# Kernel tuning notes

Measured on AMD Instinct MI355X. Metric: run time of the kernel, lower is better.

Reference implementation:

```python
import jax, jax.numpy as jnp
import numpy as np

B, N, E = 8, 64, 192
D_IN, D_PROJ = 1024, 256
F = 16            # cfg.NGM.GNN_FEAT per layer
SK_TAU = 0.05     # cfg.NGM.SK_TAU
SK_ITERS = 10
BIN_ITERS = 10
NN = N * N


def _project(x, Wp, bp, gamma, beta):
    # self.projection: Linear(1024,256) -> BatchNorm1d(256) (batch stats) -> ReLU
    B_, M, _ = x.shape
    h = x.reshape(B_ * M, -1) @ Wp + bp
    mu = h.mean(0)
    var = h.var(0)
    h = (h - mu) / jnp.sqrt(var + 1e-5) * gamma + beta
    return jax.nn.relu(h).reshape(B_, M, -1)


def _l2n(x):
    return x / jnp.clip(jnp.linalg.norm(x, axis=-1, keepdims=True), 1e-12)


def _log_sinkhorn(log_s, iters):
    for _ in range(iters):
        log_s = log_s - jax.nn.logsumexp(log_s, axis=2, keepdims=True)
        log_s = log_s - jax.nn.logsumexp(log_s, axis=1, keepdims=True)
    return jnp.exp(log_s)


def _build_K(Ke, Kp, s1, d1, s2, d2):
    # construct_sparse_aff_mat: K[a2*N+a1, b2*N+b1] += Ke[e1, e2]
    rows = s2[None, :] * N + s1[:, None]      # [E, E]
    cols = d2[None, :] * N + d1[:, None]      # [E, E]
    flat = (rows.astype(jnp.int32) * NN + cols.astype(jnp.int32)).ravel()
    K = jnp.zeros((NN * NN,), Ke.dtype).at[flat].add(Ke.ravel()).reshape(NN, NN)
    diag = jnp.arange(NN)
    # diagonal holds vec(Kp^T) (ordering a2*N + a1, matching emb = Kp.T.reshape(-1,1))
    return K.at[diag, diag].set(Kp.T.ravel())


def setup_inputs() -> dict:
    key = jax.random.key(0)
    ks = jax.random.split(key, 32)
    inp = {}
    inp['x1'] = jax.random.normal(ks[0], (B, N, D_IN), jnp.float32)
    inp['x2'] = jax.random.normal(ks[1], (B, N, D_IN), jnp.float32)
    inp['e1'] = jax.random.normal(ks[2], (B, E, D_IN), jnp.float32)
    inp['e2'] = jax.random.normal(ks[3], (B, E, D_IN), jnp.float32)
    inp['Wp'] = jax.random.normal(ks[4], (D_IN, D_PROJ), jnp.float32) * 0.02
    inp['bp'] = jnp.zeros((D_PROJ,), jnp.float32)
    inp['gamma'] = jnp.ones((D_PROJ,), jnp.float32)
    inp['beta'] = jnp.zeros((D_PROJ,), jnp.float32)
    in_dims = [1, F + 1, F + 1]
    for i, din in enumerate(in_dims):
        inp[f'W{i}'] = jax.random.normal(ks[5 + 3 * i], (din, F), jnp.float32) * 0.2
        inp[f'b{i}'] = jnp.zeros((F,), jnp.float32)
        inp[f'S{i}'] = jax.random.normal(ks[6 + 3 * i], (F, 1), jnp.float32) * 0.2
        inp[f'c{i}'] = jnp.zeros((1,), jnp.float32)
    inp['Wc'] = jax.random.normal(ks[20], (F + 1, 1), jnp.float32) * 0.2
    inp['bc'] = jnp.zeros((1,), jnp.float32)
    inp['bin_value'] = jnp.ones((1,), jnp.float32) * 0.2
    inp['src1'] = jax.random.randint(ks[21], (B, E), 0, N, jnp.int32)
    inp['dst1'] = jax.random.randint(ks[22], (B, E), 0, N, jnp.int32)
    inp['src2'] = jax.random.randint(ks[23], (B, E), 0, N, jnp.int32)
    inp['dst2'] = jax.random.randint(ks[24], (B, E), 0, N, jnp.int32)
    return inp


def reference(x1, x2, e1, e2, Wp, bp, gamma, beta,
              W0, b0, S0, c0, W1, b1, S1, c1, W2, b2, S2, c2,
              Wc, bc, bin_value, src1, dst1, src2, dst2):
    # unary / quadratic affinities via projected, L2-normalized inner products
    p1 = _project(x1, Wp, bp, gamma, beta)
    p2 = _project(x2, Wp, bp, gamma, beta)
    q1 = _project(e1, Wp, bp, gamma, beta)
    q2 = _project(e2, Wp, bp, gamma, beta)
    Kp = jnp.einsum('bnd,bmd->bnm', _l2n(p1), _l2n(p2))        # [B, N1, N2]
    Ke = 0.5 * jnp.einsum('bed,bfd->bef', _l2n(q1), _l2n(q2))  # [B, E1, E2]
    # sparse Kronecker affinity assembled densely (association graph adjacency)
    K = jax.vmap(_build_K)(Ke, Kp, src1, dst1, src2, dst2)     # [B, NN, NN]
    A = (K > 0).astype(K.dtype)
    deg = jnp.clip(A.sum(-1), 1.0)                              # [B, NN]
    x = Kp.transpose(0, 2, 1).reshape(B, NN, 1)                 # emb = vec(Kp^T)
    for (W, b, S, c) in ((W0, b0, S0, c0), (W1, b1, S1, c1), (W2, b2, S2, c2)):
        msg = jnp.einsum('bij,bjc->bic', K, x) / deg[..., None]  # sparse matvec (memory-bound)
        h = jax.nn.relu(msg @ W + b)                             # [B, NN, F]
        v = (h @ S + c).reshape(B, N, N)                         # row order a2*N+a1 -> [B, N2, N1]
        ss = _log_sinkhorn(v.transpose(0, 2, 1) / SK_TAU, SK_ITERS)  # Sinkhorn embedding channel
        x = jnp.concatenate([h, ss.transpose(0, 2, 1).reshape(B, NN, 1)], -1)
    v = (x @ Wc + bc).reshape(B, N, N)
    s = v.transpose(0, 2, 1)                                    # [B, N1, N2]
    # BinSinkhorn: pad with learned bin value, dual normalization, strip bin
    binv = bin_value[0]
    ls = jnp.concatenate([s, jnp.full((B, 1, N), binv, s.dtype)], 1)
    ls = jnp.concatenate([ls, jnp.full((B, N + 1, 1), binv, s.dtype)], 2)
    P = _log_sinkhorn(ls, BIN_ITERS)
    ss = P[:, :N, :N]
    return ss / jax.lax.stop_gradient(ss.max())
```

## Files before the change

### kernel.cpp

```cpp
#include <hip/hip_runtime.h>

constexpr int kB   = 8;
constexpr int kN   = 64;
constexpr int kE   = 192;
constexpr int kDin = 1024;
constexpr int kDp  = 256;
constexpr int kNN  = 4096;
constexpr float kTauInv = 20.0f;
constexpr int kXS  = 16;

typedef float vfloat4 __attribute__((ext_vector_type(4)));

struct SmemGemm { float As[2][16][68]; float Ws[2][16][68]; };
struct SmemCsr  {
    int km1[4096], km2[4096];
    short es1[kE], es2[kE], rp1[kE], rp2[kE];
    int cnt1[64], cnt2[64], pos1[64], pos2[64];
    int ccnt1[kE], ccnt2[kE], cpos1[kE], cpos2[kE];
};
union __align__(16) SmemK1 { SmemGemm g; SmemCsr csr; };

__global__ __launch_bounds__(256) void k_projcsr(
    const float* __restrict__ x1, const float* __restrict__ x2,
    const float* __restrict__ e1, const float* __restrict__ e2,
    const float* __restrict__ Wp,
    const int* __restrict__ src1, const int* __restrict__ dst1,
    const int* __restrict__ src2, const int* __restrict__ dst2,
    float* __restrict__ P, float* __restrict__ stats,
    int* __restrict__ off1, int* __restrict__ off2,
    int* __restrict__ lst1, int* __restrict__ lst2,
    int* __restrict__ rep1g, int* __restrict__ rep2g,
    int* __restrict__ coff1, int* __restrict__ coff2,
    int* __restrict__ clst1, int* __restrict__ clst2)
{
    const int bid = blockIdx.x, t = threadIdx.x;
    __shared__ SmemK1 u;

    if (bid < 1024) {
        const int xcd = bid & 7;
        const int ct = (bid >> 3) & 3;
        const int p = (bid >> 5) * 8 + xcd;
        const int z = p >> 6;
        const int rt = p & 63;
        const int grow0 = rt * 64, col0 = ct * 64;
        const float* src; int lrow0;
        if (rt < 8)       { src = x1; lrow0 = grow0; }
        else if (rt < 16) { src = x2; lrow0 = grow0 - 512; }
        else if (rt < 40) { src = e1; lrow0 = grow0 - 1024; }
        else              { src = e2; lrow0 = grow0 - 2560; }

        const int tx = t & 15, ty = t >> 4;
        const int arow = t >> 2, acol = (t & 3) * 4;
        const int wrow = t >> 4, wcol = (t & 15) * 4;

        const float* Abase = src + (size_t)(lrow0 + arow) * kDin + z * 256 + acol;
        const float* Wbase = Wp + (size_t)(z * 256 + wrow) * kDp + col0 + wcol;

        float4 a4 = *(const float4*)Abase;
        float4 w4 = *(const float4*)Wbase;
        float acc[4][4] = {};

        for (int c = 0; c < 16; ++c) {
            const int cur = c & 1;
            u.g.As[cur][acol + 0][arow] = a4.x;
            u.g.As[cur][acol + 1][arow] = a4.y;
            u.g.As[cur][acol + 2][arow] = a4.z;
            u.g.As[cur][acol + 3][arow] = a4.w;
            *(float4*)&u.g.Ws[cur][wrow][wcol] = w4;
            __syncthreads();
            if (c < 15) {
                a4 = *(const float4*)(Abase + (c + 1) * 16);
                w4 = *(const float4*)(Wbase + (size_t)(c + 1) * 16 * kDp);
            }
#pragma unroll
            for (int kk = 0; kk < 16; ++kk) {
                float4 av = *(const float4*)&u.g.As[cur][kk][ty * 4];
                float4 wv = *(const float4*)&u.g.Ws[cur][kk][tx * 4];
                float a[4] = {av.x, av.y, av.z, av.w};
                float w[4] = {wv.x, wv.y, wv.z, wv.w};
#pragma unroll
                for (int i = 0; i < 4; ++i)
#pragma unroll
                    for (int j = 0; j < 4; ++j)
                        acc[i][j] += a[i] * w[j];
            }
        }
        float* Pz = P + (size_t)z * 1048576;
#pragma unroll
        for (int i = 0; i < 4; ++i) {
            const int row = grow0 + ty * 4 + i;
            float4 v;
            v.x = acc[i][0]; v.y = acc[i][1]; v.z = acc[i][2]; v.w = acc[i][3];
            *(float4*)&Pz[(size_t)row * kDp + col0 + tx * 4] = v;
        }
    } else {
        const int b = bid - 1024;
        auto& C = u.csr;
        if (b == 0)
            for (int i = t; i < 2048; i += 256) stats[i] = 0.f;
        for (int i = t; i < 4096; i += 256) {
            C.km1[i] = 0x7fffffff; C.km2[i] = 0x7fffffff;
        }
        if (t < 64) { C.cnt1[t] = 0; C.cnt2[t] = 0; }
        for (int i = t; i < kE; i += 256) { C.ccnt1[i] = 0; C.ccnt2[i] = 0; }
        __syncthreads();
        if (t < kE) {
            int v1 = src1[b * kE + t], v2 = src2[b * kE + t];
            C.es1[t] = (short)v1; C.es2[t] = (short)v2;
            atomicAdd(&C.cnt1[v1], 1);
            atomicAdd(&C.cnt2[v2], 1);
            atomicMin(&C.km1[v1 * 64 + dst1[b * kE + t]], t);
            atomicMin(&C.km2[v2 * 64 + dst2[b * kE + t]], t);
        }
        __syncthreads();
        if (t < kE) {
            int r1 = C.km1[C.es1[t] * 64 + dst1[b * kE + t]];
            int r2 = C.km2[C.es2[t] * 64 + dst2[b * kE + t]];
            C.rp1[t] = (short)r1; C.rp2[t] = (short)r2;
            rep1g[b * kE + t] = r1; rep2g[b * kE + t] = r2;
            atomicAdd(&C.ccnt1[r1], 1);
            atomicAdd(&C.ccnt2[r2], 1);
        }
        __syncthreads();
        if (t == 0) {
            int a = 0, c = 0;
            for (int v = 0; v < 64; ++v) { C.pos1[v] = a; a += C.cnt1[v]; C.pos2[v] = c; c += C.cnt2[v]; }
            a = 0; c = 0;
            for (int v = 0; v < kE; ++v) { C.cpos1[v] = a; a += C.ccnt1[v]; C.cpos2[v] = c; c += C.ccnt2[v]; }
        }
        __syncthreads();
        if (t < 64) { off1[b * 65 + t] = C.pos1[t]; off2[b * 65 + t] = C.pos2[t]; }
        if (t == 0) { off1[b * 65 + 64] = kE; off2[b * 65 + 64] = kE; }
        if (t < kE) { coff1[b * 193 + t] = C.cpos1[t]; coff2[b * 193 + t] = C.cpos2[t]; }
        if (t == 0) { coff1[b * 193 + kE] = kE; coff2[b * 193 + kE] = kE; }
        __syncthreads();
        if (t < kE) {
            int p = atomicAdd(&C.pos1[C.es1[t]], 1); lst1[b * kE + p] = t;
            int q = atomicAdd(&C.pos2[C.es2[t]], 1); lst2[b * kE + q] = t;
            int cp = atomicAdd(&C.cpos1[C.rp1[t]], 1); clst1[b * kE + cp] = t;
            int cq = atomicAdd(&C.cpos2[C.rp2[t]], 1); clst2[b * kE + cq] = t;
        }
    }
}

__global__ __launch_bounds__(256) void k_reduce(
    const float* __restrict__ P, const float* __restrict__ bp,
    float* __restrict__ hbuf, float* __restrict__ stats)
{
    const int t = threadIdx.x;
    const int r0 = blockIdx.x * 16;
    const int seg = (r0 < 512) ? 0 : (r0 < 1024 ? 1 : (r0 < 2560 ? 2 : 3));
    const float bb = bp[t];
    float s = 0.f, s2 = 0.f;
#pragma unroll
    for (int rr = 0; rr < 16; ++rr) {
        size_t o = (size_t)(r0 + rr) * kDp + t;
        float v = P[o] + P[o + 1048576] + P[o + 2097152] + P[o + 3145728] + bb;
        hbuf[o] = v;
        s += v; s2 += v * v;
    }
    atomicAdd(&stats[seg * 512 + t], s);
    atomicAdd(&stats[seg * 512 + 256 + t], s2);
}

struct __align__(16) SmemSim  {
    float Xs[32][36]; float Ys[32][36];
    float muX[256], isX[256], muY[256], isY[256];
    float ga[256], be[256];
    float scX[32], scY[32];
};

__global__ __launch_bounds__(256) void k_sim(
    const float* __restrict__ hbuf, const float* __restrict__ stats,
    const float* __restrict__ gamma, const float* __restrict__ beta,
    float* __restrict__ Kp, float* __restrict__ Ke,
    int* __restrict__ bars)
{
    const int bid = blockIdx.x, t = threadIdx.x;
    __shared__ SmemSim u;

    if (bid == 0 && t == 0) { bars[3584] = 0; bars[3600] = 0; }

    const int id = bid % 40, b = bid / 40;
    int mt, nt_, ldo, segX, segY, xrow0, yrow0; float* outp; float scale;
    if (id < 4) {
        mt = (id >> 1) * 32; nt_ = (id & 1) * 32; ldo = 64;
        xrow0 = b * 64; yrow0 = 512 + b * 64;
        segX = 0; segY = 1;
        outp = Kp + (size_t)b * 4096; scale = 1.0f;
    } else {
        int e = id - 4;
        mt = (e / 6) * 32; nt_ = (e % 6) * 32; ldo = 192;
        xrow0 = 1024 + b * 192; yrow0 = 2560 + b * 192;
        segX = 2; segY = 3;
        outp = Ke + (size_t)b * 36864; scale = 0.5f;
    }
    {
        const float n = (segX < 2) ? 512.f : 1536.f;
        float mu = stats[segX * 512 + t] / n;
        float var = stats[segX * 512 + 256 + t] / n - mu * mu;
        u.muX[t] = mu; u.isX[t] = rsqrtf(var + 1e-5f);
        mu = stats[segY * 512 + t] / n;
        var = stats[segY * 512 + 256 + t] / n - mu * mu;
        u.muY[t] = mu; u.isY[t] = rsqrtf(var + 1e-5f);
        u.ga[t] = gamma[t]; u.be[t] = beta[t];
    }
    __syncthreads();
    {
        const int ri = t >> 2, lane = t & 3;
        const bool isXr = ri < 32;
        const int grow = isXr ? (xrow0 + mt + ri) : (yrow0 + nt_ + (ri - 32));
        const float* mus = isXr ? u.muX : u.muY;
        const float* iss = isXr ? u.isX : u.isY;
        const float* hr = hbuf + (size_t)grow * kDp;
        float ss = 0.f;
        for (int c4 = 0; c4 < 16; ++c4) {
            int c = lane * 64 + c4 * 4;
            float4 v = *(const float4*)&hr[c];
            float p;
            p = fmaxf((v.x - mus[c+0]) * iss[c+0] * u.ga[c+0] + u.be[c+0], 0.f); ss += p * p;
            p = fmaxf((v.y - mus[c+1]) * iss[c+1] * u.ga[c+1] + u.be[c+1], 0.f); ss += p * p;
            p = fmaxf((v.z - mus[c+2]) * iss[c+2] * u.ga[c+2] + u.be[c+2], 0.f); ss += p * p;
            p = fmaxf((v.w - mus[c+3]) * iss[c+3] * u.ga[c+3] + u.be[c+3], 0.f); ss += p * p;
        }
        ss += __shfl_xor(ss, 1);
        ss += __shfl_xor(ss, 2);
        if (lane == 0) {
            float sc = 1.f / fmaxf(sqrtf(ss), 1e-12f);
            if (isXr) u.scX[ri] = sc; else u.scY[ri - 32] = sc;
        }
    }
    __syncthreads();
    const int row = t >> 3, kq = t & 7;
    const int ty = t >> 4, tx = t & 15;
    const float* Xp = hbuf + (size_t)(xrow0 + mt) * kDp;
    const float* Yp = hbuf + (size_t)(yrow0 + nt_) * kDp;
    float acc[2][2] = {};
    for (int k0 = 0; k0 < kDp; k0 += 32) {
        const int c = k0 + kq * 4;
        float4 xa = *(const float4*)(Xp + (size_t)row * kDp + c);
        float4 ya = *(const float4*)(Yp + (size_t)row * kDp + c);
        const float sx = u.scX[row], sy = u.scY[row];
        u.Xs[kq*4+0][row] = fmaxf((xa.x - u.muX[c+0]) * u.isX[c+0] * u.ga[c+0] + u.be[c+0], 0.f) * sx;
        u.Xs[kq*4+1][row] = fmaxf((xa.y - u.muX[c+1]) * u.isX[c+1] * u.ga[c+1] + u.be[c+1], 0.f) * sx;
        u.Xs[kq*4+2][row] = fmaxf((xa.z - u.muX[c+2]) * u.isX[c+2] * u.ga[c+2] + u.be[c+2], 0.f) * sx;
        u.Xs[kq*4+3][row] = fmaxf((xa.w - u.muX[c+3]) * u.isX[c+3] * u.ga[c+3] + u.be[c+3], 0.f) * sx;
        u.Ys[kq*4+0][row] = fmaxf((ya.x - u.muY[c+0]) * u.isY[c+0] * u.ga[c+0] + u.be[c+0], 0.f) * sy;
        u.Ys[kq*4+1][row] = fmaxf((ya.y - u.muY[c+1]) * u.isY[c+1] * u.ga[c+1] + u.be[c+1], 0.f) * sy;
        u.Ys[kq*4+2][row] = fmaxf((ya.z - u.muY[c+2]) * u.isY[c+2] * u.ga[c+2] + u.be[c+2], 0.f) * sy;
        u.Ys[kq*4+3][row] = fmaxf((ya.w - u.muY[c+3]) * u.isY[c+3] * u.ga[c+3] + u.be[c+3], 0.f) * sy;
        __syncthreads();
#pragma unroll
        for (int kk = 0; kk < 32; ++kk) {
            float2 xv = *(const float2*)&u.Xs[kk][ty * 2];
            float2 yv = *(const float2*)&u.Ys[kk][tx * 2];
            acc[0][0] += xv.x * yv.x; acc[0][1] += xv.x * yv.y;
            acc[1][0] += xv.y * yv.x; acc[1][1] += xv.y * yv.y;
        }
        __syncthreads();
    }
#pragma unroll
    for (int i = 0; i < 2; ++i)
#pragma unroll
        for (int j = 0; j < 2; ++j)
            outp[(size_t)(mt + ty * 2 + i) * ldo + nt_ + tx * 2 + j] = scale * acc[i][j];
}

struct __align__(16) SmemLayer {
    float mat[64][68]; float fL[64], gL[64];
    float WL[17 * 16]; float bL[16], SL[16]; float c0v;
    float WcL[17];
    int jd2[kE]; int il[kE]; float msgT[64][18];
    int co1L[kE + 1], co2L[kE + 1];
    short cl1L[kE], cl2L[kE];
};

__device__ void sink64_local(int b, int t, float (*mat)[68], float* fL, float* gL,
                             const float* __restrict__ vin)
{
    const float4* v4 = (const float4*)(vin + b * kNN);
    for (int i = t; i < 1024; i += 256) {
        float4 v = v4[i];
        int idx = i * 4;
        int q = idx >> 6, p = idx & 63;
        mat[p][q]     = v.x * kTauInv;
        mat[p + 1][q] = v.y * kTauInv;
        mat[p + 2][q] = v.z * kTauInv;
        mat[p + 3][q] = v.w * kTauInv;
    }
    if (t < 64) { fL[t] = 0.f; gL[t] = 0.f; }
    __syncthreads();
    const int r = t >> 2, s = t & 3;
    float tv[16];
    for (int it = 0; it < 10; ++it) {
        float mx = -1e30f;
#pragma unroll
        for (int k = 0; k < 16; ++k) {
            float v = mat[r][s + 4 * k] + gL[s + 4 * k];
            tv[k] = v; mx = fmaxf(mx, v);
        }
        mx = fmaxf(mx, __shfl_xor(mx, 1));
        mx = fmaxf(mx, __shfl_xor(mx, 2));
        float sum = 0.f;
#pragma unroll
        for (int k = 0; k < 16; ++k) sum += __expf(tv[k] - mx);
        sum += __shfl_xor(sum, 1);
        sum += __shfl_xor(sum, 2);
        if (s == 0) fL[r] = -(mx + __logf(sum));
        __syncthreads();
        mx = -1e30f;
#pragma unroll
        for (int k = 0; k < 16; ++k) {
            float v = mat[s + 4 * k][r] + fL[s + 4 * k];
            tv[k] = v; mx = fmaxf(mx, v);
        }
        mx = fmaxf(mx, __shfl_xor(mx, 1));
        mx = fmaxf(mx, __shfl_xor(mx, 2));
        sum = 0.f;
#pragma unroll
        for (int k = 0; k < 16; ++k) sum += __expf(tv[k] - mx);
        sum += __shfl_xor(sum, 1);
        sum += __shfl_xor(sum, 2);
        if (s == 0) gL[r] = -(mx + __logf(sum));
        __syncthreads();
    }
    const float fr = fL[r];
#pragma unroll
    for (int k = 0; k < 16; ++k) {
        int q = s + 4 * k;
        mat[r][q] = __expf(mat[r][q] + fr + gL[q]);
    }
    __syncthreads();
}

template <int C, bool LASTP>
__device__ void layer_body(int bid, int t, SmemLayer& L,
    const int* __restrict__ off1, const int* __restrict__ lst1,
    const int* __restrict__ off2, const int* __restrict__ lst2,
    const int* __restrict__ d1, const int* __restrict__ d2,
    const int* __restrict__ rep1g, const int* __restrict__ rep2g,
    const int* __restrict__ coff1, const int* __restrict__ coff2,
    const int* __restrict__ clst1, const int* __restrict__ clst2,
    const float* __restrict__ Ke, const float* __restrict__ x,
    const float* __restrict__ Kp, int* __restrict__ degcnt,
    const float* __restrict__ W, const float* __restrict__ bb,
    const float* __restrict__ S, const float* __restrict__ c0,
    const float* __restrict__ Wc,
    const float* __restrict__ vprev, float* __restrict__ xn,
    float* __restrict__ vcbuf, float* __restrict__ vout)
{
    const int b = bid & 7, r2 = bid >> 3;
    for (int k = t; k < C * 16; k += 256) L.WL[k] = W[k];
    if (t < 16) { L.bL[t] = bb[t]; L.SL[t] = S[t]; }
    if (t == 0) L.c0v = c0[0];
    if (LASTP && t < 17) L.WcL[t] = Wc[t];
    const int j0 = off2[b * 65 + r2];
    const int n2 = off2[b * 65 + r2 + 1] - j0;
    for (int k = t; k < n2; k += 256) {
        int j = lst2[b * kE + j0 + k];
        int v = (j << 8) | d2[b * kE + j];
        if (C == 1 && rep2g[b * kE + j] == j) v |= 1 << 16;
        L.jd2[k] = v;
    }
    for (int k = t; k < kE; k += 256) {
        int i = lst1[b * kE + k];
        int v = (i << 8) | d1[b * kE + i];
        if (C == 1 && rep1g[b * kE + i] == i) v |= 1 << 16;
        L.il[k] = v;
    }
    if constexpr (C == 1) {
        for (int k = t; k < kE + 1; k += 256) {
            L.co1L[k] = coff1[b * 193 + k];
            L.co2L[k] = coff2[b * 193 + k];
        }
        for (int k = t; k < kE; k += 256) {
            L.cl1L[k] = (short)clst1[b * kE + k];
            L.cl2L[k] = (short)clst2[b * kE + k];
        }
    }
    if constexpr (C == 17) {
        sink64_local(b, t, L.mat, L.fL, L.gL, vprev);
    } else {
        __syncthreads();
    }

    const int r1 = t >> 2, lane = t & 3;
    const int i0 = off1[b * 65 + r1], i1 = off1[b * 65 + r1 + 1];
    const float* Keb = Ke + (size_t)b * kE * kE;
    const float* KpB = Kp + (size_t)b * kNN;
    int degLocal = 0;

    if constexpr (C == 1) {
        float acc = 0.f;
        for (int k = 0; k < n2; ++k) {
            int pk = L.jd2[k], j = (pk >> 8) & 255, dd2 = pk & 255;
            for (int m = i0 + lane; m < i1; m += 4) {
                int pi = L.il[m], i = (pi >> 8) & 255, dd1 = pi & 255;
                if (dd2 == r2 && dd1 == r1) continue;
                acc += Keb[(size_t)i * kE + j] * KpB[dd1 * 64 + dd2];
            }
        }
        acc += __shfl_xor(acc, 1);
        acc += __shfl_xor(acc, 2);
        if (lane == 0) L.msgT[r1][0] = acc;
        for (int m = i0 + lane; m < i1; m += 4) {
            int pi = L.il[m];
            if (!(pi >> 16)) continue;
            int i = (pi >> 8) & 255, dd1 = pi & 255;
            for (int k = 0; k < n2; ++k) {
                int pk = L.jd2[k];
                if (!(pk >> 16)) continue;
                int j = (pk >> 8) & 255, dd2 = pk & 255;
                float sum = 0.f;
                for (int mm = L.co1L[i]; mm < L.co1L[i + 1]; ++mm) {
                    const float* kr = Keb + (size_t)L.cl1L[mm] * kE;
                    for (int nn = L.co2L[j]; nn < L.co2L[j + 1]; ++nn)
                        sum += kr[L.cl2L[nn]];
                }
                if ((r2 * 64 + r1) != (dd2 * 64 + dd1) && sum > 0.0f) ++degLocal;
            }
        }
        degLocal += __shfl_xor(degLocal, 1);
        degLocal += __shfl_xor(degLocal, 2);
    } else {
        const float* xb = x + (size_t)b * kNN * kXS;
        float acc[5];
#pragma unroll
        for (int cc = 0; cc < 5; ++cc) acc[cc] = 0.f;
        for (int k = 0; k < n2; ++k) {
            int pk = L.jd2[k], j = (pk >> 8) & 255, dd2 = pk & 255;
            const float* xrow = xb + (size_t)(dd2 * 64) * kXS;
            for (int m = i0; m < i1; ++m) {
                int pi = L.il[m], dd1 = pi & 255;
                if (dd2 == r2 && dd1 == r1) continue;
                int i = (pi >> 8) & 255;
                float kv = Keb[(size_t)i * kE + j];
                float4 xv = *(const float4*)(xrow + dd1 * kXS + lane * 4);
                acc[0] += kv * xv.x;
                acc[1] += kv * xv.y;
                acc[2] += kv * xv.z;
                acc[3] += kv * xv.w;
                if (lane == 0) acc[4] += kv * L.mat[dd1][dd2];
            }
        }
#pragma unroll
        for (int q = 0; q < 4; ++q)
            L.msgT[r1][lane * 4 + q] = acc[q];
        if (lane == 0) L.msgT[r1][16] = acc[4];
    }
    __syncthreads();

    const int row = r2 * 64 + r1;
    const int idx = b * kNN + row;
    const float kd = KpB[r1 * 64 + r2];
    int degv;
    if constexpr (C == 1) {
        degv = degLocal;
        if (lane == 0) degcnt[idx] = degLocal;
    } else {
        degv = degcnt[idx];
    }
    const float dg = fmaxf((float)(degv + (kd > 0.f ? 1 : 0)), 1.f);
    float m[C];
    if constexpr (C == 1) {
        m[0] = (L.msgT[r1][0] + kd * kd) / dg;
    } else {
        float4 xa  = *(const float4*)(x + (size_t)idx * kXS + 0);
        float4 xb4 = *(const float4*)(x + (size_t)idx * kXS + 4);
        float4 xc4 = *(const float4*)(x + (size_t)idx * kXS + 8);
        float4 xd4 = *(const float4*)(x + (size_t)idx * kXS + 12);
        m[0]  = (L.msgT[r1][0]  + kd * xa.x) / dg;
        m[1]  = (L.msgT[r1][1]  + kd * xa.y) / dg;
        m[2]  = (L.msgT[r1][2]  + kd * xa.z) / dg;
        m[3]  = (L.msgT[r1][3]  + kd * xa.w) / dg;
        m[4]  = (L.msgT[r1][4]  + kd * xb4.x) / dg;
        m[5]  = (L.msgT[r1][5]  + kd * xb4.y) / dg;
        m[6]  = (L.msgT[r1][6]  + kd * xb4.z) / dg;
        m[7]  = (L.msgT[r1][7]  + kd * xb4.w) / dg;
        m[8]  = (L.msgT[r1][8]  + kd * xc4.x) / dg;
        m[9]  = (L.msgT[r1][9]  + kd * xc4.y) / dg;
        m[10] = (L.msgT[r1][10] + kd * xc4.z) / dg;
        m[11] = (L.msgT[r1][11] + kd * xc4.w) / dg;
        m[12] = (L.msgT[r1][12] + kd * xd4.x) / dg;
        m[13] = (L.msgT[r1][13] + kd * xd4.y) / dg;
        m[14] = (L.msgT[r1][14] + kd * xd4.z) / dg;
        m[15] = (L.msgT[r1][15] + kd * xd4.w) / dg;
        m[16] = (L.msgT[r1][16] + kd * L.mat[r1][r2]) / dg;
    }
    float h[4];
    float vpart = 0.f;
#pragma unroll
    for (int ff = 0; ff < 4; ++ff) {
        int f = lane * 4 + ff;
        float a = L.bL[f];
#pragma unroll
        for (int c = 0; c < C; ++c) a += m[c] * L.WL[c * 16 + f];
        h[ff] = fmaxf(a, 0.f);
        vpart += h[ff] * L.SL[f];
    }
    if constexpr (!LASTP) {
        float4 hv; hv.x = h[0]; hv.y = h[1]; hv.z = h[2]; hv.w = h[3];
        *(float4*)(xn + (size_t)idx * kXS + lane * 4) = hv;
    } else {
        float vcp = h[0] * L.WcL[lane * 4 + 0] + h[1] * L.WcL[lane * 4 + 1]
                  + h[2] * L.WcL[lane * 4 + 2] + h[3] * L.WcL[lane * 4 + 3];
        vcp += __shfl_xor(vcp, 1);
        vcp += __shfl_xor(vcp, 2);
        if (lane == 0) vcbuf[idx] = vcp;
    }
    vpart += __shfl_xor(vpart, 1);
    vpart += __shfl_xor(vpart, 2);
    if (lane == 0) vout[idx] = vpart + L.c0v;
}

__global__ __launch_bounds__(256) void k_l0(
    const int* __restrict__ off1, const int* __restrict__ lst1,
    const int* __restrict__ off2, const int* __restrict__ lst2,
    const int* __restrict__ dst1, const int* __restrict__ dst2,
    const int* __restrict__ rep1g, const int* __restrict__ rep2g,
    const int* __restrict__ coff1, const int* __restrict__ coff2,
    const int* __restrict__ clst1, const int* __restrict__ clst2,
    const float* __restrict__ Ke, const float* __restrict__ Kp,
    int* __restrict__ degcnt,
    const float* __restrict__ W0, const float* __restrict__ b0,
    const float* __restrict__ S0, const float* __restrict__ c0,
    float* __restrict__ xA, float* __restrict__ vA)
{
    __shared__ SmemLayer L;
    layer_body<1, false>(blockIdx.x, threadIdx.x, L,
        off1, lst1, off2, lst2, dst1, dst2, rep1g, rep2g,
        coff1, coff2, clst1, clst2, Ke, nullptr, Kp, degcnt,
        W0, b0, S0, c0, nullptr, nullptr, xA, nullptr, vA);
}

__global__ __launch_bounds__(256) void k_l1(
    const int* __restrict__ off1, const int* __restrict__ lst1,
    const int* __restrict__ off2, const int* __restrict__ lst2,
    const int* __restrict__ dst1, const int* __restrict__ dst2,
    const float* __restrict__ Ke, const float* __restrict__ Kp,
    int* __restrict__ degcnt,
    const float* __restrict__ W1, const float* __restrict__ b1,
    const float* __restrict__ S1, const float* __restrict__ c1,
    const float* __restrict__ xA, const float* __restrict__ vA,
    float* __restrict__ xB, float* __restrict__ vB)
{
    __shared__ SmemLayer L;
    layer_body<17, false>(blockIdx.x, threadIdx.x, L,
        off1, lst1, off2, lst2, dst1, dst2, nullptr, nullptr,
        nullptr, nullptr, nullptr, nullptr, Ke, xA, Kp, degcnt,
        W1, b1, S1, c1, nullptr, vA, xB, nullptr, vB);
}

__global__ __launch_bounds__(256) void k_l2(
    const int* __restrict__ off1, const int* __restrict__ lst1,
    const int* __restrict__ off2, const int* __restrict__ lst2,
    const int* __restrict__ dst1, const int* __restrict__ dst2,
    const float* __restrict__ Ke, const float* __restrict__ Kp,
    int* __restrict__ degcnt,
    const float* __restrict__ W2, const float* __restrict__ b2,
    const float* __restrict__ S2, const float* __restrict__ c2,
    const float* __restrict__ Wc,
    const float* __restrict__ xB, const float* __restrict__ vB,
    float* __restrict__ vcbuf, float* __restrict__ vA)
{
    __shared__ SmemLayer L;
    layer_body<17, true>(blockIdx.x, threadIdx.x, L,
        off1, lst1, off2, lst2, dst1, dst2, nullptr, nullptr,
        nullptr, nullptr, nullptr, nullptr, Ke, xB, Kp, degcnt,
        W2, b2, S2, c2, Wc, vB, nullptr, vcbuf, vA);
}

struct __align__(16) SmemSinkF {
    float mat[65][68]; float fL[72], gL[72];
    float wred[9];
};

__global__ __launch_bounds__(576) void k_final(
    const float* __restrict__ vA, const float* __restrict__ vcbuf,
    const float* __restrict__ Wc, const float* __restrict__ bc,
    const float* __restrict__ binv,
    int* __restrict__ bars, float* __restrict__ out)
{
    const int b = blockIdx.x, t = threadIdx.x;
    __shared__ SmemSinkF S;

    for (int i = t; i < kNN; i += 576) {
        int q = i >> 6, p = i & 63;
        S.mat[p][q] = vA[b * kNN + i] * kTauInv;
    }
    if (t < 72) { S.fL[t] = 0.f; S.gL[t] = 0.f; }
    __syncthreads();

    const int r = t >> 3, s = t & 7;

    {
        const bool act = r < 64;
        const int rr = act ? r : 0;
        float Lr[8], Lc[8], tv[8];
#pragma unroll
        for (int k = 0; k < 8; ++k) {
            Lr[k] = S.mat[rr][s + 8 * k];
            Lc[k] = S.mat[s + 8 * k][rr];
        }
        __syncthreads();
        for (int it = 0; it < 10; ++it) {
            float mx = -1e30f;
#pragma unroll
            for (int k = 0; k < 8; ++k) { tv[k] = Lr[k] + S.gL[s + 8 * k]; mx = fmaxf(mx, tv[k]); }
            mx = fmaxf(mx, __shfl_xor(mx, 1));
            mx = fmaxf(mx, __shfl_xor(mx, 2));
            mx = fmaxf(mx, __shfl_xor(mx, 4));
            float sum = 0.f;
#pragma unroll
            for (int k = 0; k < 8; ++k) sum += __expf(tv[k] - mx);
            sum += __shfl_xor(sum, 1);
            sum += __shfl_xor(sum, 2);
            sum += __shfl_xor(sum, 4);
            if (act && s == 0) S.fL[r] = -(mx + __logf(sum));
            __syncthreads();
            mx = -1e30f;
#pragma unroll
            for (int k = 0; k < 8; ++k) { tv[k] = Lc[k] + S.fL[s + 8 * k]; mx = fmaxf(mx, tv[k]); }
            mx = fmaxf(mx, __shfl_xor(mx, 1));
            mx = fmaxf(mx, __shfl_xor(mx, 2));
            mx = fmaxf(mx, __shfl_xor(mx, 4));
            sum = 0.f;
#pragma unroll
            for (int k = 0; k < 8; ++k) sum += __expf(tv[k] - mx);
            sum += __shfl_xor(sum, 1);
            sum += __shfl_xor(sum, 2);
            sum += __shfl_xor(sum, 4);
            if (act && s == 0) S.gL[r] = -(mx + __logf(sum));
            __syncthreads();
        }
        if (act) {
            const float fr = S.fL[r];
#pragma unroll
            for (int k = 0; k < 8; ++k) {
                int q = s + 8 * k;
                S.mat[r][q] = __expf(Lr[k] + fr + S.gL[q]);
            }
        }
    }
    __syncthreads();

    {
        const float Wc16 = Wc[16], bcv = bc[0], binvv = binv[0];
        const float* vcb = vcbuf + (size_t)b * kNN;
        for (int idx = t; idx < 65 * 65; idx += 576) {
            int q = idx / 65, p = idx - q * 65;
            float v;
            if (p < 64 && q < 64)
                v = vcb[q * 64 + p] + S.mat[p][q] * Wc16 + bcv;
            else v = binvv;
            S.mat[p][q] = v;
        }
        if (t < 72) { S.fL[t] = 0.f; S.gL[t] = 0.f; }
    }
    __syncthreads();

    const bool act = r < 65;
    const int rr = act ? r : 0;
    float Lrow[9], Lcol[9], tv[9];
#pragma unroll
    for (int k = 0; k < 8; ++k) {
        Lrow[k] = S.mat[rr][s + 8 * k];
        Lcol[k] = S.mat[s + 8 * k][rr];
    }
    Lrow[8] = (s == 0) ? S.mat[rr][64] : -1e30f;
    Lcol[8] = (s == 0) ? S.mat[64][rr] : -1e30f;
    __syncthreads();

    for (int it = 0; it < 10; ++it) {
        float mx = -1e30f;
#pragma unroll
        for (int k = 0; k < 9; ++k) { tv[k] = Lrow[k] + S.gL[s + 8 * k]; mx = fmaxf(mx, tv[k]); }
        mx = fmaxf(mx, __shfl_xor(mx, 1));
        mx = fmaxf(mx, __shfl_xor(mx, 2));
        mx = fmaxf(mx, __shfl_xor(mx, 4));
        float sum = 0.f;
#pragma unroll
        for (int k = 0; k < 9; ++k) sum += __expf(tv[k] - mx);
        sum += __shfl_xor(sum, 1);
        sum += __shfl_xor(sum, 2);
        sum += __shfl_xor(sum, 4);
        if (act && s == 0) S.fL[r] = -(mx + __logf(sum));
        __syncthreads();
        mx = -1e30f;
#pragma unroll
        for (int k = 0; k < 9; ++k) { tv[k] = Lcol[k] + S.fL[s + 8 * k]; mx = fmaxf(mx, tv[k]); }
        mx = fmaxf(mx, __shfl_xor(mx, 1));
        mx = fmaxf(mx, __shfl_xor(mx, 2));
        mx = fmaxf(mx, __shfl_xor(mx, 4));
        sum = 0.f;
#pragma unroll
        for (int k = 0; k < 9; ++k) sum += __expf(tv[k] - mx);
        sum += __shfl_xor(sum, 1);
        sum += __shfl_xor(sum, 2);
        sum += __shfl_xor(sum, 4);
        if (act && s == 0) S.gL[r] = -(mx + __logf(sum));
        __syncthreads();
    }

    float ev[8];
    float lmax = 0.f;
    if (r < 64) {
        const float fr = S.fL[r];
#pragma unroll
        for (int k = 0; k < 8; ++k) {
            ev[k] = __expf(Lrow[k] + fr + S.gL[s + 8 * k]);
            lmax = fmaxf(lmax, ev[k]);
        }
    }
#pragma unroll
    for (int o = 32; o >= 1; o >>= 1) lmax = fmaxf(lmax, __shfl_xor(lmax, o));
    if ((t & 63) == 0) S.wred[t >> 6] = lmax;
    __syncthreads();
    int* mcnt = bars + 3584;
    int* gmax = bars + 3600;
    if (t == 0) {
        float mb = S.wred[0];
#pragma unroll
        for (int w = 1; w < 9; ++w) mb = fmaxf(mb, S.wred[w]);
        atomicMax(gmax, __float_as_int(mb));
        asm volatile("s_waitcnt vmcnt(0)" ::: "memory");
        __hip_atomic_fetch_add(mcnt, 1, __ATOMIC_RELAXED, __HIP_MEMORY_SCOPE_AGENT);
        while (__hip_atomic_load(mcnt, __ATOMIC_RELAXED, __HIP_MEMORY_SCOPE_AGENT) < 8)
            __builtin_amdgcn_s_sleep(2);
    }
    __syncthreads();
    const float inv = 1.f / __int_as_float(
        __hip_atomic_load(gmax, __ATOMIC_RELAXED, __HIP_MEMORY_SCOPE_AGENT));
    if (r < 64) {
#pragma unroll
        for (int k = 0; k < 8; ++k)
            out[((size_t)b * kN + r) * kN + s + 8 * k] = ev[k] * inv;
    }
}

extern "C" void kernel_launch(void* const* d_in, const int* in_sizes, int n_in,
                              void* d_out, int out_size, void* d_ws, size_t ws_size,
                              hipStream_t stream)
{
    (void)in_sizes; (void)n_in; (void)out_size; (void)ws_size;

    const float* x1    = (const float*)d_in[0];
    const float* x2    = (const float*)d_in[1];
    const float* e1    = (const float*)d_in[2];
    const float* e2    = (const float*)d_in[3];
    const float* Wp    = (const float*)d_in[4];
    const float* bp    = (const float*)d_in[5];
    const float* gamma = (const float*)d_in[6];
    const float* beta  = (const float*)d_in[7];
    const float* W0 = (const float*)d_in[8];
    const float* b0 = (const float*)d_in[9];
    const float* S0 = (const float*)d_in[10];
    const float* c0 = (const float*)d_in[11];
    const float* W1 = (const float*)d_in[12];
    const float* b1 = (const float*)d_in[13];
    const float* S1 = (const float*)d_in[14];
    const float* c1 = (const float*)d_in[15];
    const float* W2 = (const float*)d_in[16];
    const float* b2 = (const float*)d_in[17];
    const float* S2 = (const float*)d_in[18];
    const float* c2 = (const float*)d_in[19];
    const float* Wc = (const float*)d_in[20];
    const float* bc = (const float*)d_in[21];
    const float* binv = (const float*)d_in[22];
    const int* src1 = (const int*)d_in[23];
    const int* dst1 = (const int*)d_in[24];
    const int* src2 = (const int*)d_in[25];
    const int* dst2 = (const int*)d_in[26];

    float* out = (float*)d_out;
    float* wsf = (float*)d_ws;

    float* hbuf  = wsf;
    float* P     = hbuf + 1048576;
    float* Kp    = P + 4194304;
    float* Ke    = Kp + 32768;
    float* vA    = Ke + 294912;
    float* vB    = vA + 32768;
    float* xA    = vB + 32768;
    float* xB    = xA + 524288;
    float* vcbuf = xB + 524288;
    int*   degcnt = (int*)(vcbuf + 32768);
    int*   off1 = degcnt + 32768;
    int*   off2 = off1 + 520;
    int*   lst1 = off2 + 520;
    int*   lst2 = lst1 + 1536;
    int*   rep1g = lst2 + 1536;
    int*   rep2g = rep1g + 1536;
    int*   coff1 = rep2g + 1536;
    int*   coff2 = coff1 + 1544;
    int*   clst1 = coff2 + 1544;
    int*   clst2 = clst1 + 1536;
    float* stats = (float*)(clst2 + 1536);
    int*   bars  = (int*)(stats + 2048);

    k_projcsr<<<dim3(1032), dim3(256), 0, stream>>>(
        x1, x2, e1, e2, Wp, src1, dst1, src2, dst2, P, stats,
        off1, off2, lst1, lst2, rep1g, rep2g, coff1, coff2, clst1, clst2);
    k_reduce<<<dim3(256), dim3(256), 0, stream>>>(P, bp, hbuf, stats);
    k_sim<<<dim3(320), dim3(256), 0, stream>>>(hbuf, stats, gamma, beta, Kp, Ke, bars);
    k_l0<<<dim3(512), dim3(256), 0, stream>>>(
        off1, lst1, off2, lst2, dst1, dst2, rep1g, rep2g,
        coff1, coff2, clst1, clst2, Ke, Kp, degcnt,
        W0, b0, S0, c0, xA, vA);
    k_l1<<<dim3(512), dim3(256), 0, stream>>>(
        off1, lst1, off2, lst2, dst1, dst2, Ke, Kp, degcnt,
        W1, b1, S1, c1, xA, vA, xB, vB);
    k_l2<<<dim3(512), dim3(256), 0, stream>>>(
        off1, lst1, off2, lst2, dst1, dst2, Ke, Kp, degcnt,
        W2, b2, S2, c2, Wc, xB, vB, vcbuf, vA);
    k_final<<<dim3(8), dim3(576), 0, stream>>>(vA, vcbuf, Wc, bc, binv, bars, out);
}
```

Before: 288.9 us.

## Fuse final Sinkhorn into last layer kernel via last-block-per-batch counter

Removes the separate k_final launch. Each k_l2 block bumps a per-batch atomic counter, and the last of the 64 blocks for a batch runs the embedding Sinkhorn plus the bin Sinkhorn and writes the output. Writes to vA and vcbuf become agent-scope atomic stores and are read back with atomic loads so other blocks' results are visible. This saves one launch and the gap between kernels. In exchange, the finalize now runs on 256 threads instead of 576, and the spin barrier across 8 finalizing blocks assumes those blocks are all resident at once.

```diff
diff --git a/kernel.cpp b/kernel.cpp
--- a/kernel.cpp
+++ b/kernel.cpp
@@ -10,6 +10,16 @@
 constexpr int kXS  = 16;
 
 typedef float vfloat4 __attribute__((ext_vector_type(4)));
+
+__device__ __forceinline__ float cload(const float* p) {
+    return __hip_atomic_load(p, __ATOMIC_RELAXED, __HIP_MEMORY_SCOPE_AGENT);
+}
+__device__ __forceinline__ void cstore(float* p, float v) {
+    __hip_atomic_store(p, v, __ATOMIC_RELAXED, __HIP_MEMORY_SCOPE_AGENT);
+}
+__device__ __forceinline__ void cstorei(int* p, int v) {
+    __hip_atomic_store(p, v, __ATOMIC_RELAXED, __HIP_MEMORY_SCOPE_AGENT);
+}
 
 struct SmemGemm { float As[2][16][68]; float Ws[2][16][68]; };
 struct SmemCsr  {
@@ -179,7 +189,12 @@
     const int bid = blockIdx.x, t = threadIdx.x;
     __shared__ SmemSim u;
 
-    if (bid == 0 && t == 0) { bars[3584] = 0; bars[3600] = 0; }
+    if (bid == 0 && t == 0) {
+        cstorei(&bars[3584], 0);
+        cstorei(&bars[3600], 0);
+        for (int i = 0; i < 8; ++i)
+            cstorei(&bars[3616 + i * 16], 0);
+    }
 
     const int id = bid % 40, b = bid / 40;
     int mt, nt_, ldo, segX, segY, xrow0, yrow0; float* outp; float scale;
@@ -273,6 +288,13 @@
     int jd2[kE]; int il[kE]; float msgT[64][18];
     int co1L[kE + 1], co2L[kE + 1];
     short cl1L[kE], cl2L[kE];
+};
+struct __align__(16) SmemSinkF {
+    float mat[65][68]; float fL[68], gL[68]; float wred[4];
+};
+struct __align__(16) SmemL2 {
+    union { SmemLayer ly; SmemSinkF sk; } u;
+    int isLast;
 };
 
 __device__ void sink64_local(int b, int t, float (*mat)[68], float* fL, float* gL,
@@ -506,11 +528,14 @@
                   + h[2] * L.WcL[lane * 4 + 2] + h[3] * L.WcL[lane * 4 + 3];
         vcp += __shfl_xor(vcp, 1);
         vcp += __shfl_xor(vcp, 2);
-        if (lane == 0) vcbuf[idx] = vcp;
+        if (lane == 0) cstore(&vcbuf[idx], vcp);
     }
     vpart += __shfl_xor(vpart, 1);
     vpart += __shfl_xor(vpart, 2);
-    if (lane == 0) vout[idx] = vpart + L.c0v;
+    if (lane == 0) {
+        if (LASTP) cstore(&vout[idx], vpart + L.c0v);
+        else       vout[idx] = vpart + L.c0v;
+    }
 }
 
 __global__ __launch_bounds__(256) void k_l0(
@@ -551,6 +576,177 @@
         W1, b1, S1, c1, nullptr, vA, xB, nullptr, vB);
 }
 
+__device__ void finalize(int b, int t, SmemSinkF& S,
+    const float* __restrict__ vA, const float* __restrict__ vcbuf,
+    const float* __restrict__ Wc, const float* __restrict__ bc,
+    const float* __restrict__ binv,
+    int* __restrict__ bars, float* __restrict__ out)
+{
+    for (int i = t; i < kNN; i += 256) {
+        int q = i >> 6, p = i & 63;
+        S.mat[p][q] = cload(&vA[b * kNN + i]) * kTauInv;
+    }
+    if (t < 68) { S.fL[t] = 0.f; S.gL[t] = 0.f; }
+    __syncthreads();
+    const int r = t >> 2, s = t & 3;
+    {
+        float tv[16];
+        for (int it = 0; it < 10; ++it) {
+            float mx = -1e30f;
+#pragma unroll
+            for (int k = 0; k < 16; ++k) {
+                float v = S.mat[r][s + 4 * k] + S.gL[s + 4 * k];
+                tv[k] = v; mx = fmaxf(mx, v);
+            }
+            mx = fmaxf(mx, __shfl_xor(mx, 1));
+            mx = fmaxf(mx, __shfl_xor(mx, 2));
+            float sum = 0.f;
+#pragma unroll
+            for (int k = 0; k < 16; ++k) sum += __expf(tv[k] - mx);
+            sum += __shfl_xor(sum, 1);
+            sum += __shfl_xor(sum, 2);
+            if (s == 0) S.fL[r] = -(mx + __logf(sum));
+            __syncthreads();
+            mx = -1e30f;
+#pragma unroll
+            for (int k = 0; k < 16; ++k) {
+                float v = S.mat[s + 4 * k][r] + S.fL[s + 4 * k];
+                tv[k] = v; mx = fmaxf(mx, v);
+            }
+            mx = fmaxf(mx, __shfl_xor(mx, 1));
+            mx = fmaxf(mx, __shfl_xor(mx, 2));
+            sum = 0.f;
+#pragma unroll
+            for (int k = 0; k < 16; ++k) sum += __expf(tv[k] - mx);
+            sum += __shfl_xor(sum, 1);
+            sum += __shfl_xor(sum, 2);
+            if (s == 0) S.gL[r] = -(mx + __logf(sum));
+            __syncthreads();
+        }
+        const float fr = S.fL[r];
+#pragma unroll
+        for (int k = 0; k < 16; ++k) {
+            int q = s + 4 * k;
+            S.mat[r][q] = __expf(S.mat[r][q] + fr + S.gL[q]);
+        }
+    }
+    __syncthreads();
+
+    {
+        const float Wc16 = Wc[16], bcv = bc[0], binvv = binv[0];
+        for (int idx = t; idx < 65 * 65; idx += 256) {
+            int q = idx / 65, p = idx - q * 65;
+            float v;
+            if (p < 64 && q < 64)
+                v = cload(&vcbuf[b * kNN + q * 64 + p]) + S.mat[p][q] * Wc16 + bcv;
+            else v = binvv;
+            S.mat[p][q] = v;
+        }
+        if (t < 68) { S.fL[t] = 0.f; S.gL[t] = 0.f; }
+    }
+    __syncthreads();
+
+    float Lrow[17], Lcol[17];
+#pragma unroll
+    for (int k = 0; k < 17; ++k) {
+        int q = s + 4 * k;
+        Lrow[k] = (q <= 64) ? S.mat[r][q] : -1e30f;
+        Lcol[k] = (q <= 64) ? S.mat[q][r] : -1e30f;
+    }
+    float tv[17], tv2[17];
+    for (int it = 0; it < 10; ++it) {
+        float mx = -1e30f;
+#pragma unroll
+        for (int k = 0; k < 17; ++k) { tv[k] = Lrow[k] + S.gL[s + 4 * k]; mx = fmaxf(mx, tv[k]); }
+        mx = fmaxf(mx, __shfl_xor(mx, 1));
+        mx = fmaxf(mx, __shfl_xor(mx, 2));
+        float sum = 0.f;
+#pragma unroll
+        for (int k = 0; k < 17; ++k) sum += __expf(tv[k] - mx);
+        sum += __shfl_xor(sum, 1);
+        sum += __shfl_xor(sum, 2);
+        if (s == 0) S.fL[r] = -(mx + __logf(sum));
+        if (r == 0) {
+            float mx2 = -1e30f;
+#pragma unroll
+            for (int k = 0; k < 17; ++k) {
+                int q = s + 4 * k;
+                tv2[k] = (q <= 64) ? S.mat[64][q] + S.gL[q] : -1e30f;
+                mx2 = fmaxf(mx2, tv2[k]);
+            }
+            mx2 = fmaxf(mx2, __shfl_xor(mx2, 1));
+            mx2 = fmaxf(mx2, __shfl_xor(mx2, 2));
+            float sum2 = 0.f;
+#pragma unroll
+            for (int k = 0; k < 17; ++k) sum2 += __expf(tv2[k] - mx2);
+            sum2 += __shfl_xor(sum2, 1);
+            sum2 += __shfl_xor(sum2, 2);
+            if (s == 0) S.fL[64] = -(mx2 + __logf(sum2));
+        }
+        __syncthreads();
+        mx = -1e30f;
+#pragma unroll
+        for (int k = 0; k < 17; ++k) { tv[k] = Lcol[k] + S.fL[s + 4 * k]; mx = fmaxf(mx, tv[k]); }
+        mx = fmaxf(mx, __shfl_xor(mx, 1));
+        mx = fmaxf(mx, __shfl_xor(mx, 2));
+        sum = 0.f;
+#pragma unroll
+        for (int k = 0; k < 17; ++k) sum += __expf(tv[k] - mx);
+        sum += __shfl_xor(sum, 1);
+        sum += __shfl_xor(sum, 2);
+        if (s == 0) S.gL[r] = -(mx + __logf(sum));
+        if (r == 0) {
+            float mx2 = -1e30f;
+#pragma unroll
+            for (int k = 0; k < 17; ++k) {
+                int p = s + 4 * k;
+                tv2[k] = (p <= 64) ? S.mat[p][64] + S.fL[p] : -1e30f;
+                mx2 = fmaxf(mx2, tv2[k]);
+            }
+            mx2 = fmaxf(mx2, __shfl_xor(mx2, 1));
+            mx2 = fmaxf(mx2, __shfl_xor(mx2, 2));
+            float sum2 = 0.f;
+#pragma unroll
+            for (int k = 0; k < 17; ++k) sum2 += __expf(tv2[k] - mx2);
+            sum2 += __shfl_xor(sum2, 1);
+            sum2 += __shfl_xor(sum2, 2);
+            if (s == 0) S.gL[64] = -(mx2 + __logf(sum2));
+        }
+        __syncthreads();
+    }
+
+    float ev[16];
+    float lmax = 0.f;
+    {
+        const float fr = S.fL[r];
+#pragma unroll
+        for (int k = 0; k < 16; ++k) {
+            ev[k] = __expf(Lrow[k] + fr + S.gL[s + 4 * k]);
+            lmax = fmaxf(lmax, ev[k]);
+        }
+    }
+#pragma unroll
+    for (int o = 32; o >= 1; o >>= 1) lmax = fmaxf(lmax, __shfl_xor(lmax, o));
+    if ((t & 63) == 0) S.wred[t >> 6] = lmax;
+    __syncthreads();
+    int* mcnt = bars + 3584;
+    int* gmax = bars + 3600;
+    if (t == 0) {
+        float mb = fmaxf(fmaxf(S.wred[0], S.wred[1]), fmaxf(S.wred[2], S.wred[3]));
+        atomicMax(gmax, __float_as_int(mb));
+        asm volatile("s_waitcnt vmcnt(0)" ::: "memory");
+        __hip_atomic_fetch_add(mcnt, 1, __ATOMIC_RELAXED, __HIP_MEMORY_SCOPE_AGENT);
+        while (__hip_atomic_load(mcnt, __ATOMIC_RELAXED, __HIP_MEMORY_SCOPE_AGENT) < 8)
+            __builtin_amdgcn_s_sleep(2);
+    }
+    __syncthreads();
+    const float inv = 1.f / __int_as_float(
+        __hip_atomic_load(gmax, __ATOMIC_RELAXED, __HIP_MEMORY_SCOPE_AGENT));
+#pragma unroll
+    for (int k = 0; k < 16; ++k)
+        out[((size_t)b * kN + r) * kN + s + 4 * k] = ev[k] * inv;
+}
+
 __global__ __launch_bounds__(256) void k_l2(
     const int* __restrict__ off1, const int* __restrict__ lst1,
     const int* __restrict__ off2, const int* __restrict__ lst2,
@@ -559,183 +755,30 @@
     int* __restrict__ degcnt,
     const float* __restrict__ W2, const float* __restrict__ b2,
     const float* __restrict__ S2, const float* __restrict__ c2,
-    const float* __restrict__ Wc,
+    const float* __restrict__ Wc, const float* __restrict__ bc,
+    const float* __restrict__ binv,
     const float* __restrict__ xB, const float* __restrict__ vB,
-    float* __restrict__ vcbuf, float* __restrict__ vA)
-{
-    __shared__ SmemLayer L;
-    layer_body<17, true>(blockIdx.x, threadIdx.x, L,
+    float* __restrict__ vcbuf, float* __restrict__ vA,
+    int* __restrict__ bars, float* __restrict__ out)
+{
+    const int bid = blockIdx.x, t = threadIdx.x;
+    __shared__ SmemL2 M;
+    layer_body<17, true>(bid, t, M.u.ly,
         off1, lst1, off2, lst2, dst1, dst2, nullptr, nullptr,
         nullptr, nullptr, nullptr, nullptr, Ke, xB, Kp, degcnt,
         W2, b2, S2, c2, Wc, vB, nullptr, vcbuf, vA);
-}
-
-struct __align__(16) SmemSinkF {
-    float mat[65][68]; float fL[72], gL[72];
-    float wred[9];
-};
-
-__global__ __launch_bounds__(576) void k_final(
-    const float* __restrict__ vA, const float* __restrict__ vcbuf,
-    const float* __restrict__ Wc, const float* __restrict__ bc,
-    const float* __restrict__ binv,
-    int* __restrict__ bars, float* __restrict__ out)
-{
-    const int b = blockIdx.x, t = threadIdx.x;
-    __shared__ SmemSinkF S;
-
-    for (int i = t; i < kNN; i += 576) {
-        int q = i >> 6, p = i & 63;
-        S.mat[p][q] = vA[b * kNN + i] * kTauInv;
-    }
-    if (t < 72) { S.fL[t] = 0.f; S.gL[t] = 0.f; }
-    __syncthreads();
-
-    const int r = t >> 3, s = t & 7;
-
-    {
-        const bool act = r < 64;
-        const int rr = act ? r : 0;
-        float Lr[8], Lc[8], tv[8];
-#pragma unroll
-        for (int k = 0; k < 8; ++k) {
-            Lr[k] = S.mat[rr][s + 8 * k];
-            Lc[k] = S.mat[s + 8 * k][rr];
-        }
-        __syncthreads();
-        for (int it = 0; it < 10; ++it) {
-            float mx = -1e30f;
-#pragma unroll
-            for (int k = 0; k < 8; ++k) { tv[k] = Lr[k] + S.gL[s + 8 * k]; mx = fmaxf(mx, tv[k]); }
-            mx = fmaxf(mx, __shfl_xor(mx, 1));
-            mx = fmaxf(mx, __shfl_xor(mx, 2));
-            mx = fmaxf(mx, __shfl_xor(mx, 4));
-            float sum = 0.f;
-#pragma unroll
-            for (int k = 0; k < 8; ++k) sum += __expf(tv[k] - mx);
-            sum += __shfl_xor(sum, 1);
-            sum += __shfl_xor(sum, 2);
-            sum += __shfl_xor(sum, 4);
-            if (act && s == 0) S.fL[r] = -(mx + __logf(sum));
-            __syncthreads();
-            mx = -1e30f;
-#pragma unroll
-            for (int k = 0; k < 8; ++k) { tv[k] = Lc[k] + S.fL[s + 8 * k]; mx = fmaxf(mx, tv[k]); }
-            mx = fmaxf(mx, __shfl_xor(mx, 1));
-            mx = fmaxf(mx, __shfl_xor(mx, 2));
-            mx = fmaxf(mx, __shfl_xor(mx, 4));
-            sum = 0.f;
-#pragma unroll
-            for (int k = 0; k < 8; ++k) sum += __expf(tv[k] - mx);
-            sum += __shfl_xor(sum, 1);
-            sum += __shfl_xor(sum, 2);
-            sum += __shfl_xor(sum, 4);
-            if (act && s == 0) S.gL[r] = -(mx + __logf(sum));
-            __syncthreads();
-        }
-        if (act) {
-            const float fr = S.fL[r];
-#pragma unroll
-            for (int k = 0; k < 8; ++k) {
-                int q = s + 8 * k;
-                S.mat[r][q] = __expf(Lr[k] + fr + S.gL[q]);
-            }
-        }
-    }
-    __syncthreads();
-
-    {
-        const float Wc16 = Wc[16], bcv = bc[0], binvv = binv[0];
-        const float* vcb = vcbuf + (size_t)b * kNN;
-        for (int idx = t; idx < 65 * 65; idx += 576) {
-            int q = idx / 65, p = idx - q * 65;
-            float v;
-            if (p < 64 && q < 64)
-                v = vcb[q * 64 + p] + S.mat[p][q] * Wc16 + bcv;
-            else v = binvv;
-            S.mat[p][q] = v;
-        }
-        if (t < 72) { S.fL[t] = 0.f; S.gL[t] = 0.f; }
-    }
-    __syncthreads();
-
-    const bool act = r < 65;
-    const int rr = act ? r : 0;
-    float Lrow[9], Lcol[9], tv[9];
-#pragma unroll
-    for (int k = 0; k < 8; ++k) {
-        Lrow[k] = S.mat[rr][s + 8 * k];
-        Lcol[k] = S.mat[s + 8 * k][rr];
-    }
-    Lrow[8] = (s == 0) ? S.mat[rr][64] : -1e30f;
-    Lcol[8] = (s == 0) ? S.mat[64][rr] : -1e30f;
-    __syncthreads();
-
-    for (int it = 0; it < 10; ++it) {
-        float mx = -1e30f;
-#pragma unroll
-        for (int k = 0; k < 9; ++k) { tv[k] = Lrow[k] + S.gL[s + 8 * k]; mx = fmaxf(mx, tv[k]); }
-        mx = fmaxf(mx, __shfl_xor(mx, 1));
-        mx = fmaxf(mx, __shfl_xor(mx, 2));
-        mx = fmaxf(mx, __shfl_xor(mx, 4));
-        float sum = 0.f;
-#pragma unroll
-        for (int k = 0; k < 9; ++k) sum += __expf(tv[k] - mx);
-        sum += __shfl_xor(sum, 1);
-        sum += __shfl_xor(sum, 2);
-        sum += __shfl_xor(sum, 4);
-        if (act && s == 0) S.fL[r] = -(mx + __logf(sum));
-        __syncthreads();
-        mx = -1e30f;
-#pragma unroll
-        for (int k = 0; k < 9; ++k) { tv[k] = Lcol[k] + S.fL[s + 8 * k]; mx = fmaxf(mx, tv[k]); }
-        mx = fmaxf(mx, __shfl_xor(mx, 1));
-        mx = fmaxf(mx, __shfl_xor(mx, 2));
-        mx = fmaxf(mx, __shfl_xor(mx, 4));
-        sum = 0.f;
-#pragma unroll
-        for (int k = 0; k < 9; ++k) sum += __expf(tv[k] - mx);
-        sum += __shfl_xor(sum, 1);
-        sum += __shfl_xor(sum, 2);
-        sum += __shfl_xor(sum, 4);
-        if (act && s == 0) S.gL[r] = -(mx + __logf(sum));
-        __syncthreads();
-    }
-
-    float ev[8];
-    float lmax = 0.f;
-    if (r < 64) {
-        const float fr = S.fL[r];
-#pragma unroll
-        for (int k = 0; k < 8; ++k) {
-            ev[k] = __expf(Lrow[k] + fr + S.gL[s + 8 * k]);
-            lmax = fmaxf(lmax, ev[k]);
-        }
-    }
-#pragma unroll
-    for (int o = 32; o >= 1; o >>= 1) lmax = fmaxf(lmax, __shfl_xor(lmax, o));
-    if ((t & 63) == 0) S.wred[t >> 6] = lmax;
-    __syncthreads();
-    int* mcnt = bars + 3584;
-    int* gmax = bars + 3600;
+
+    asm volatile("s_waitcnt vmcnt(0)" ::: "memory");
+    __syncthreads();
+    const int b = bid & 7;
     if (t == 0) {
-        float mb = S.wred[0];
-#pragma unroll
-        for (int w = 1; w < 9; ++w) mb = fmaxf(mb, S.wred[w]);
-        atomicMax(gmax, __float_as_int(mb));
-        asm volatile("s_waitcnt vmcnt(0)" ::: "memory");
-        __hip_atomic_fetch_add(mcnt, 1, __ATOMIC_RELAXED, __HIP_MEMORY_SCOPE_AGENT);
-        while (__hip_atomic_load(mcnt, __ATOMIC_RELAXED, __HIP_MEMORY_SCOPE_AGENT) < 8)
-            __builtin_amdgcn_s_sleep(2);
-    }
-    __syncthreads();
-    const float inv = 1.f / __int_as_float(
-        __hip_atomic_load(gmax, __ATOMIC_RELAXED, __HIP_MEMORY_SCOPE_AGENT));
-    if (r < 64) {
-#pragma unroll
-        for (int k = 0; k < 8; ++k)
-            out[((size_t)b * kN + r) * kN + s + 8 * k] = ev[k] * inv;
-    }
+        int prev = __hip_atomic_fetch_add(&bars[3616 + b * 16], 1,
+                                          __ATOMIC_RELAXED, __HIP_MEMORY_SCOPE_AGENT);
+        M.isLast = (prev == 63);
+    }
+    __syncthreads();
+    if (!M.isLast) return;
+    finalize(b, t, M.u.sk, vA, vcbuf, Wc, bc, binv, bars, out);
 }
 
 extern "C" void kernel_launch(void* const* d_in, const int* in_sizes, int n_in,
@@ -812,6 +855,5 @@
         W1, b1, S1, c1, xA, vA, xB, vB);
     k_l2<<<dim3(512), dim3(256), 0, stream>>>(
         off1, lst1, off2, lst2, dst1, dst2, Ke, Kp, degcnt,
-        W2, b2, S2, c2, Wc, xB, vB, vcbuf, vA);
-    k_final<<<dim3(8), dim3(576), 0, stream>>>(vA, vcbuf, Wc, bc, binv, bars, out);
-}
+        W2, b2, S2, c2, Wc, bc, binv, xB, vB, vcbuf, vA, bars, out);
+}
```

After: 304.5 us. 5.4% more time.
